# Kernel optimization log

Measured on AMD Instinct MI355X. Metric: run time of the kernel, lower is better.

The kernel has to match this reference:

```python
import jax, jax.numpy as jnp
import numpy as np
import math

B, S, H, NH = 8, 1024, 1024, 16
DH = H // NH


def _ln(x, g, b, eps=1e-5):
    m = x.mean(-1, keepdims=True)
    v = ((x - m) ** 2).mean(-1, keepdims=True)
    return (x - m) / jnp.sqrt(v + eps) * g + b


def _attn(qx, kx, vx, wq, bq, wk, bk, wv, bv, wo, bo, mask):
    b = qx.shape[0]
    def heads(t, w, bias):
        return (t @ w + bias).reshape(b, -1, NH, DH).transpose(0, 2, 1, 3)
    q, k, v = heads(qx, wq, bq), heads(kx, wk, bk), heads(vx, wv, bv)
    corr = jnp.einsum('bhqd,bhkd->bhqk', q, k) / math.sqrt(DH)  # [B,NH,Sq,Sk]
    corr = jnp.where(mask[:, None, :, None] == 0, -1e9, corr)  # mask per query row
    p = jax.nn.softmax(corr, axis=-1)
    o = jnp.einsum('bhqk,bhkd->bhqd', p, v).transpose(0, 2, 1, 3).reshape(b, -1, H)
    return o @ wo + bo


def setup_inputs() -> dict:
    key = jax.random.key(0)
    ks = jax.random.split(key, 16)
    d = {}
    d['x'] = jax.random.normal(ks[0], (B, S, H), jnp.float32)
    d['h'] = jax.random.normal(ks[1], (B, S, H), jnp.float32)
    d['mask'] = jnp.ones((B, S), jnp.int32)
    wnames = ['sa_wq', 'sa_wk', 'sa_wv', 'sa_wo', 'ca_wq', 'ca_wk', 'ca_wv', 'ca_wo', 'ff_w1', 'ff_w2']
    for i, n in enumerate(wnames):
        d[n] = jax.random.normal(ks[2 + i], (H, H), jnp.float32) * 0.02
    for n in ['sa_bq', 'sa_bk', 'sa_bv', 'sa_bo', 'ca_bq', 'ca_bk', 'ca_bv', 'ca_bo', 'ff_b1', 'ff_b2']:
        d[n] = jnp.zeros((H,), jnp.float32)
    for n in ['ln1', 'ln2', 'ln3', 'lnh', 'ff_ln']:
        d[n + '_g'] = jnp.ones((H,), jnp.float32)
        d[n + '_b'] = jnp.zeros((H,), jnp.float32)
    return d


def reference(x, h, mask, ln1_g, ln1_b, ln2_g, ln2_b, ln3_g, ln3_b, lnh_g, lnh_b,
              sa_wq, sa_bq, sa_wk, sa_bk, sa_wv, sa_bv, sa_wo, sa_bo,
              ca_wq, ca_bq, ca_wk, ca_bk, ca_wv, ca_bv, ca_wo, ca_bo,
              ff_w1, ff_b1, ff_w2, ff_b2, ff_ln_g, ff_ln_b):
    # self-attention block (pre-LN, residual)
    xn = _ln(x, ln1_g, ln1_b)
    hidden_in = _attn(xn, xn, xn, sa_wq, sa_bq, sa_wk, sa_bk, sa_wv, sa_bv, sa_wo, sa_bo, mask) + x
    # cross-attention block
    mid_n = _ln(hidden_in, ln2_g, ln2_b)
    hn = _ln(h, lnh_g, lnh_b)
    hidden_mid = _attn(mid_n, hn, hn, ca_wq, ca_bq, ca_wk, ca_bk, ca_wv, ca_bv, ca_wo, ca_bo, mask) + hidden_in
    # position-wise FFN (Conv1d k=1 == pointwise linear) with its own LN+residual
    y = _ln(hidden_mid, ln3_g, ln3_b)
    ff = jax.nn.relu(y @ ff_w1 + ff_b1) @ ff_w2 + ff_b2
    ffo = _ln(ff + y, ff_ln_g, ff_ln_b)
    return ffo + hidden_mid
```

## Files before the change

kernel.cpp:

```cpp
#include <hip/hip_runtime.h>

typedef unsigned short u16;
typedef unsigned int u32;
typedef float f32x4 __attribute__((ext_vector_type(4)));
typedef float f32x16 __attribute__((ext_vector_type(16)));
typedef __bf16 bf16x8 __attribute__((ext_vector_type(8)));

#define MFMA16(a, b, c) __builtin_amdgcn_mfma_f32_16x16x32_bf16(a, b, c, 0, 0, 0)
#define MFMA32(a, b, c) __builtin_amdgcn_mfma_f32_32x32x16_bf16(a, b, c, 0, 0, 0)
#define PLSWAP(x, y) asm volatile("v_permlane32_swap_b32 %0, %1" : "+v"(x), "+v"(y))

__device__ __forceinline__ u16 f2b(float f) {
    u32 u = __builtin_bit_cast(u32, f);
    u += 0x7fffu + ((u >> 16) & 1u);
    return (u16)(u >> 16);
}

__device__ __forceinline__ u32 pk2(float a, float b) {
    union { u32 u; __bf16 h[2]; } r;
    r.h[0] = (__bf16)a; r.h[1] = (__bf16)b;
    return r.u;
}

__device__ __forceinline__ void gload16(const u16* g, u16* l) {
    __builtin_amdgcn_global_load_lds((const __attribute__((address_space(1))) void*)g,
                                     (__attribute__((address_space(3))) void*)l, 16, 0, 0);
}

struct W10 { const float* p[10]; };
__global__ __launch_bounds__(256) void tcvt_k(W10 wp, u16* __restrict__ WT0) {
    const float* __restrict__ Wm = wp.p[blockIdx.z];
    u16* __restrict__ WT = WT0 + (size_t)blockIdx.z * 1048576;
    __shared__ float t[32][33];
    int bx = blockIdx.x, by = blockIdx.y;
    int tx = threadIdx.x, ty = threadIdx.y;
#pragma unroll
    for (int j = 0; j < 32; j += 8)
        t[ty + j][tx] = Wm[(size_t)(by * 32 + ty + j) * 1024 + bx * 32 + tx];
    __syncthreads();
#pragma unroll
    for (int j = 0; j < 32; j += 8)
        WT[(size_t)(bx * 32 + ty + j) * 1024 + by * 32 + tx] = f2b(t[tx][ty + j]);
}

__global__ __launch_bounds__(256) void vtr_k(const u16* __restrict__ Vg, int ldv, u16* __restrict__ VT) {
    __shared__ u16 t[32][34];
    int bx = blockIdx.x, by = blockIdx.y, b = blockIdx.z;
    int tx = threadIdx.x, ty = threadIdx.y;
#pragma unroll
    for (int j = 0; j < 32; j += 8)
        t[ty + j][tx] = Vg[(size_t)(b * 1024 + by * 32 + ty + j) * ldv + bx * 32 + tx];
    __syncthreads();
#pragma unroll
    for (int j = 0; j < 32; j += 8)
        VT[(size_t)(b * 1024 + bx * 32 + ty + j) * 1024 + by * 32 + tx] = t[tx][ty + j];
}

template <int MODE>
__global__ __launch_bounds__(256) void ln_k(const float* __restrict__ in1, const float* __restrict__ in2,
                                            const float* __restrict__ gg, const float* __restrict__ bb,
                                            const float* __restrict__ post,
                                            float* __restrict__ of, u16* __restrict__ ob) {
    int row = blockIdx.x, tid = threadIdx.x;
    size_t base = (size_t)row * 1024 + tid * 4;
    float4 x = *(const float4*)(in1 + base);
    if constexpr (MODE & 1) {
        float4 x2 = *(const float4*)(in2 + base);
        x.x += x2.x; x.y += x2.y; x.z += x2.z; x.w += x2.w;
    }
    float s1 = x.x + x.y + x.z + x.w;
    float s2 = x.x * x.x + x.y * x.y + x.z * x.z + x.w * x.w;
#pragma unroll
    for (int m = 32; m >= 1; m >>= 1) { s1 += __shfl_xor(s1, m); s2 += __shfl_xor(s2, m); }
    __shared__ float r1[4], r2[4];
    int lane = tid & 63, w = tid >> 6;
    if (lane == 0) { r1[w] = s1; r2[w] = s2; }
    __syncthreads();
    s1 = r1[0] + r1[1] + r1[2] + r1[3];
    s2 = r2[0] + r2[1] + r2[2] + r2[3];
    float mean = s1 * (1.0f / 1024.0f);
    float var = s2 * (1.0f / 1024.0f) - mean * mean;
    float rstd = rsqrtf(var + 1e-5f);
    float4 gv = *(const float4*)(gg + tid * 4);
    float4 bv = *(const float4*)(bb + tid * 4);
    float y0 = (x.x - mean) * rstd * gv.x + bv.x;
    float y1 = (x.y - mean) * rstd * gv.y + bv.y;
    float y2 = (x.z - mean) * rstd * gv.z + bv.z;
    float y3 = (x.w - mean) * rstd * gv.w + bv.w;
    if constexpr (MODE & 2) {
        float o0 = y0, o1 = y1, o2 = y2, o3 = y3;
        if constexpr (MODE & 8) {
            float4 p = *(const float4*)(post + base);
            o0 += p.x; o1 += p.y; o2 += p.z; o3 += p.w;
        }
        float4 o; o.x = o0; o.y = o1; o.z = o2; o.w = o3;
        *(float4*)(of + base) = o;
    }
    if constexpr (MODE & 4) {
        uint2 pk;
        pk.x = (u32)f2b(y0) | ((u32)f2b(y1) << 16);
        pk.y = (u32)f2b(y2) | ((u32)f2b(y3) << 16);
        *(uint2*)(ob + base) = pk;
    }
}

template <int EPI, int NBT>
__global__ __launch_bounds__(256, 3) void gemm_k(const u16* __restrict__ A, int lda,
                                                 const u16* __restrict__ WT,
                                                 const float* __restrict__ b0, const float* __restrict__ b1,
                                                 const float* __restrict__ b2,
                                                 float sc0, float sc1, float sc2,
                                                 const float* __restrict__ res,
                                                 void* __restrict__ outp, int ldc) {
    const int K = 1024;
    __shared__ u16 aL[2][4096];
    __shared__ u16 bL[2][4096];
    int id = blockIdx.x;
    const int CPX = 64 * NBT / 8;
    int swz = (id & 7) * CPX + (id >> 3);
    int bm = swz / NBT, bn = swz % NBT;
    const int m0 = bm * 128, n0 = bn * 128;
    int tid = threadIdx.x, lane = tid & 63, w = tid >> 6;
    int wm = w >> 1, wn = w & 1;
    int col = lane & 15, g = lane >> 4;
    const u16* Ag = A + (size_t)(m0 + w * 32 + (lane >> 2)) * lda + (lane & 3) * 8;
    const u16* Bg = WT + (size_t)(n0 + w * 32 + (lane >> 2)) * K + (lane & 3) * 8;

#define STG(buf, kt)                                                                            \
    {                                                                                           \
        _Pragma("unroll") for (int i_ = 0; i_ < 2; i_++) {                                      \
            gload16(Ag + (size_t)(kt) * 32 + (size_t)i_ * 16 * lda, &aL[buf][w * 1024 + i_ * 512]); \
            gload16(Bg + (size_t)(kt) * 32 + (size_t)i_ * 16 * K, &bL[buf][w * 1024 + i_ * 512]);   \
        }                                                                                       \
    }

    f32x4 acc[4][4];
#pragma unroll
    for (int m = 0; m < 4; m++)
#pragma unroll
        for (int n = 0; n < 4; n++) acc[m][n] = (f32x4){0.f, 0.f, 0.f, 0.f};

    STG(0, 0);
    __syncthreads();
#pragma unroll 2
    for (int kt = 0; kt < 32; ++kt) {
        int cur = kt & 1;
        if (kt < 31) STG(cur ^ 1, kt + 1);
        bf16x8 af[4], bfv[4];
#pragma unroll
        for (int m = 0; m < 4; m++) af[m] = *(const bf16x8*)&aL[cur][(wm * 64 + m * 16 + col) * 32 + g * 8];
#pragma unroll
        for (int n = 0; n < 4; n++) bfv[n] = *(const bf16x8*)&bL[cur][(wn * 64 + n * 16 + col) * 32 + g * 8];
#pragma unroll
        for (int m = 0; m < 4; m++)
#pragma unroll
            for (int n = 0; n < 4; n++) acc[m][n] = MFMA16(af[m], bfv[n], acc[m][n]);
        __syncthreads();
    }
#undef STG
    int seg = n0 >> 10;
    const float* bp = (NBT == 8) ? b0 : (seg == 0 ? b0 : (seg == 1 ? b1 : b2));
    float sg = (NBT == 8) ? sc0 : (seg == 0 ? sc0 : (seg == 1 ? sc1 : sc2));
    int nseg = n0 & 1023;
    float bv[4];
#pragma unroll
    for (int n = 0; n < 4; n++) bv[n] = bp[nseg + wn * 64 + n * 16 + col];
#pragma unroll
    for (int m = 0; m < 4; m++) {
#pragma unroll
        for (int r = 0; r < 4; r++) {
            int row = m0 + wm * 64 + m * 16 + g * 4 + r;
#pragma unroll
            for (int n = 0; n < 4; n++) {
                int c = n0 + wn * 64 + n * 16 + col;
                size_t idx = (size_t)row * ldc + c;
                float v = (acc[m][n][r] + bv[n]) * sg;
                if constexpr (EPI == 0) ((u16*)outp)[idx] = f2b(v);
                else if constexpr (EPI == 1) ((u16*)outp)[idx] = f2b(fmaxf(v, 0.f));
                else if constexpr (EPI == 2) ((float*)outp)[idx] = v + res[idx];
            }
        }
    }
}

__global__ __launch_bounds__(256) void attn_k(const u16* __restrict__ Q, int ldq,
                                              const u16* __restrict__ Kc, int ldk,
                                              const u16* __restrict__ VT,
                                              const int* __restrict__ mask,
                                              u16* __restrict__ O, int ldo) {
    const int S = 1024;
    int gid = blockIdx.x;
    int bq = gid >> 7, hh = (gid >> 3) & 15, bb = gid & 7;
    int tid = threadIdx.x, lane = tid & 63, w = tid >> 6;
    int q = lane & 31, hl = lane >> 5;
    int q0w = bq * 128 + w * 32;

    __shared__ u16 sm[18432];
#define KT(b, r, c) sm[(b) * 9216 + (r) * 72 + (c)]
#define VTL(b, r, c) sm[(b) * 9216 + 4608 + (r) * 72 + (c)]

    const u16* Qrow = Q + ((size_t)bb * S + q0w + q) * ldq + hh * 64;
    bool mneg = (mask[bb * S + q0w + q] == 0);
    bf16x8 qf[4];
#pragma unroll
    for (int c = 0; c < 4; c++) {
        qf[c] = *(const bf16x8*)(Qrow + c * 16 + hl * 8);
        if (mneg) qf[c] = (bf16x8)(__bf16)0.f;
    }

    float l = 0.f;
    f32x16 oa[2];
#pragma unroll
    for (int i = 0; i < 16; i++) { oa[0][i] = 0.f; oa[1][i] = 0.f; }

    int kk = tid >> 2, ks = tid & 3;
    const u16* gK = Kc + ((size_t)bb * S + kk) * ldk + hh * 64 + ks * 16;
    const u16* gVT = VT + ((size_t)(bb * 16 + hh) * 64 + kk) * 1024 + ks * 16;
    uint4 kr0, kr1, vr0, vr1;

#define LOADT(t)                                                      \
    {                                                                 \
        const u16* pk_ = gK + (size_t)(t) * 64 * ldk;                 \
        kr0 = *(const uint4*)pk_; kr1 = *(const uint4*)(pk_ + 8);     \
        const u16* pv_ = gVT + (size_t)(t) * 64;                      \
        vr0 = *(const uint4*)pv_; vr1 = *(const uint4*)(pv_ + 8);     \
    }
#define STORET(bf)                                       \
    {                                                    \
        *(uint4*)&KT(bf, kk, ks * 16) = kr0;             \
        *(uint4*)&KT(bf, kk, ks * 16 + 8) = kr1;         \
        *(uint4*)&VTL(bf, kk, ks * 16) = vr0;            \
        *(uint4*)&VTL(bf, kk, ks * 16 + 8) = vr1;        \
    }

    LOADT(0);
    STORET(0);

    for (int t = 0; t < 16; ++t) {
        int cur = t & 1;
        if (t < 15) LOADT(t + 1);
        __syncthreads();

        f32x16 sc[2];
#pragma unroll
        for (int i = 0; i < 16; i++) { sc[0][i] = 0.f; sc[1][i] = 0.f; }
        __builtin_amdgcn_s_setprio(1);
#pragma unroll
        for (int st = 0; st < 2; st++)
#pragma unroll
            for (int c = 0; c < 4; c++) {
                bf16x8 kf = *(const bf16x8*)&KT(cur, st * 32 + q, c * 16 + hl * 8);
                sc[st] = MFMA32(kf, qf[c], sc[st]);
            }
        __builtin_amdgcn_s_setprio(0);

#pragma unroll
        for (int st = 0; st < 2; st++)
#pragma unroll
            for (int r = 0; r < 16; r++) sc[st][r] = exp2f(sc[st][r]);
        float ts[8];
#pragma unroll
        for (int i = 0; i < 8; i++)
            ts[i] = (sc[0][i] + sc[0][i + 8]) + (sc[1][i] + sc[1][i + 8]);
#pragma unroll
        for (int i = 0; i < 4; i++) ts[i] += ts[i + 4];
        float rs = (ts[0] + ts[2]) + (ts[1] + ts[3]);
        rs += __shfl_xor(rs, 32);
        l += rs;

        __builtin_amdgcn_s_setprio(1);
#pragma unroll
        for (int st = 0; st < 2; st++) {
            u32 wv[8];
#pragma unroll
            for (int j = 0; j < 8; j++) wv[j] = pk2(sc[st][2 * j], sc[st][2 * j + 1]);
            PLSWAP(wv[0], wv[2]); PLSWAP(wv[1], wv[3]);
            PLSWAP(wv[4], wv[6]); PLSWAP(wv[5], wv[7]);
#pragma unroll
            for (int c = 0; c < 2; c++) {
                union { u32 u[4]; bf16x8 v; } pb;
                pb.u[0] = wv[c * 4 + 0]; pb.u[1] = wv[c * 4 + 1];
                pb.u[2] = wv[c * 4 + 2]; pb.u[3] = wv[c * 4 + 3];
#pragma unroll
                for (int dd = 0; dd < 2; dd++) {
                    bf16x8 vf = *(const bf16x8*)&VTL(cur, dd * 32 + q, st * 32 + c * 16 + hl * 8);
                    oa[dd] = MFMA32(vf, pb.v, oa[dd]);
                }
            }
        }
        __builtin_amdgcn_s_setprio(0);

        if (t < 15) STORET(cur ^ 1);
    }

    __syncthreads();
    float inv = 1.0f / l;
    u16* otw = sm + w * 2304;
#pragma unroll
    for (int dd = 0; dd < 2; dd++)
#pragma unroll
        for (int r = 0; r < 16; r++) {
            int d = (r & 3) + 8 * (r >> 2) + 4 * hl + 32 * dd;
            otw[q * 72 + d] = f2b(oa[dd][r] * inv);
        }
    __syncthreads();
    size_t obase = ((size_t)bb * S + q0w) * ldo + hh * 64;
#pragma unroll
    for (int i = 0; i < 4; i++) {
        int row = i * 8 + (lane >> 3);
        uint4 vdat = *(const uint4*)&otw[row * 72 + (lane & 7) * 8];
        *(uint4*)(O + obase + (size_t)row * ldo + (lane & 7) * 8) = vdat;
    }
#undef KT
#undef VTL
#undef LOADT
#undef STORET
}

extern "C" void kernel_launch(void* const* d_in, const int* in_sizes, int n_in,
                              void* d_out, int out_size, void* d_ws, size_t ws_size,
                              hipStream_t stream) {
    (void)in_sizes; (void)n_in; (void)out_size; (void)ws_size;
    const float* x = (const float*)d_in[0];
    const float* h = (const float*)d_in[1];
    const int* mask = (const int*)d_in[2];
    const float* W[10];
    const float* Bv[10];
    for (int i = 0; i < 10; i++) { W[i] = (const float*)d_in[3 + i]; Bv[i] = (const float*)d_in[13 + i]; }
    const float *ln1g = (const float*)d_in[23], *ln1b = (const float*)d_in[24];
    const float *ln2g = (const float*)d_in[25], *ln2b = (const float*)d_in[26];
    const float *ln3g = (const float*)d_in[27], *ln3b = (const float*)d_in[28];
    const float *lnhg = (const float*)d_in[29], *lnhb = (const float*)d_in[30];
    const float *flng = (const float*)d_in[31], *flnb = (const float*)d_in[32];

    const float SCLE = 0.18033688011112042f;

    char* ws = (char*)d_ws;
    size_t off = 0;
    auto alloc = [&](size_t bytes) -> char* {
        char* p = ws + off;
        off += (bytes + 255) & ~(size_t)255;
        return p;
    };
    const size_t MT = (size_t)8192 * 1024;
    u16* wtb = (u16*)alloc((size_t)10 * 1048576 * 2);
    u16* wt[10];
    for (int i = 0; i < 10; i++) wt[i] = wtb + (size_t)i * 1048576;
    u16* qkv = (u16*)alloc((size_t)8192 * 3072 * 2);
    u16* kv = qkv;
    u16* kb = qkv + (size_t)8192 * 2048;
    u16* bufA = (u16*)alloc(MT * 2);
    u16* qb   = (u16*)alloc(MT * 2);
    float* hid_in  = (float*)alloc(MT * 4);
    float* hid_mid = (float*)alloc(MT * 4);
    float* yf      = (float*)alloc(MT * 4);
    u16* hn = (u16*)yf;
    u16* vt_sa = bufA;
    u16* vt_ca = (u16*)hid_mid;
    float* outF = (float*)d_out;

    W10 wp;
    for (int i = 0; i < 10; i++) wp.p[i] = W[i];
    tcvt_k<<<dim3(32, 32, 10), dim3(32, 8), 0, stream>>>(wp, wtb);

    ln_k<4><<<8192, 256, 0, stream>>>(x, nullptr, ln1g, ln1b, nullptr, nullptr, bufA);
    gemm_k<0, 24><<<1536, 256, 0, stream>>>(bufA, 1024, wt[0], Bv[0], Bv[1], Bv[2], SCLE, 1.f, 1.f, nullptr, qkv, 3072);
    vtr_k<<<dim3(32, 32, 8), dim3(32, 8), 0, stream>>>(qkv + 2048, 3072, vt_sa);
    attn_k<<<1024, 256, 0, stream>>>(qkv, 3072, qkv + 1024, 3072, vt_sa, mask, qkv, 3072);
    gemm_k<2, 8><<<512, 256, 0, stream>>>(qkv, 3072, wt[3], Bv[3], Bv[3], Bv[3], 1.f, 1.f, 1.f, x, hid_in, 1024);

    ln_k<4><<<8192, 256, 0, stream>>>(hid_in, nullptr, ln2g, ln2b, nullptr, nullptr, bufA);
    ln_k<4><<<8192, 256, 0, stream>>>(h, nullptr, lnhg, lnhb, nullptr, nullptr, hn);
    gemm_k<0, 8><<<512, 256, 0, stream>>>(bufA, 1024, wt[4], Bv[4], Bv[4], Bv[4], SCLE, 1.f, 1.f, nullptr, qb, 1024);
    gemm_k<0, 16><<<1024, 256, 0, stream>>>(hn, 1024, wt[5], Bv[5], Bv[6], Bv[6], 1.f, 1.f, 1.f, nullptr, kv, 2048);
    vtr_k<<<dim3(32, 32, 8), dim3(32, 8), 0, stream>>>(kv + 1024, 2048, vt_ca);
    attn_k<<<1024, 256, 0, stream>>>(qb, 1024, kv, 2048, vt_ca, mask, qb, 1024);
    gemm_k<2, 8><<<512, 256, 0, stream>>>(qb, 1024, wt[7], Bv[7], Bv[7], Bv[7], 1.f, 1.f, 1.f, hid_in, hid_mid, 1024);

    ln_k<6><<<8192, 256, 0, stream>>>(hid_mid, nullptr, ln3g, ln3b, nullptr, yf, bufA);
    gemm_k<1, 8><<<512, 256, 0, stream>>>(bufA, 1024, wt[8], Bv[8], Bv[8], Bv[8], 1.f, 1.f, 1.f, nullptr, kb, 1024);
    gemm_k<2, 8><<<512, 256, 0, stream>>>(kb, 1024, wt[9], Bv[9], Bv[9], Bv[9], 1.f, 1.f, 1.f, yf, hid_in, 1024);
    ln_k<10><<<8192, 256, 0, stream>>>(hid_in, nullptr, flng, flnb, hid_mid, outF, nullptr);
}
```

Before: 495.8 us.

## Deepen GEMM pipeline to four LDS stages with swizzled layout and manual waits

The GEMM main loop moves from a double buffer to a four-slot LDS ring that keeps three k-tiles in flight. Completion is tracked with explicit vmcnt waits and raw barriers instead of __syncthreads. LDS rows are XOR-swizzled on both the global-to-LDS store and the fragment reads to cut bank conflicts, and MFMA sections get raised priority. The larger LDS footprint (64 KB) lowers the occupancy hint from 3 to 2 blocks per CU, which weakens latency hiding across blocks.

```diff
diff --git a/kernel.cpp b/kernel.cpp
--- a/kernel.cpp
+++ b/kernel.cpp
@@ -9,6 +9,14 @@
 #define MFMA16(a, b, c) __builtin_amdgcn_mfma_f32_16x16x32_bf16(a, b, c, 0, 0, 0)
 #define MFMA32(a, b, c) __builtin_amdgcn_mfma_f32_32x32x16_bf16(a, b, c, 0, 0, 0)
 #define PLSWAP(x, y) asm volatile("v_permlane32_swap_b32 %0, %1" : "+v"(x), "+v"(y))
+#define CFENCE() asm volatile("" ::: "memory")
+#define BAR()                         \
+    {                                 \
+        CFENCE();                     \
+        __builtin_amdgcn_s_barrier(); \
+        CFENCE();                     \
+    }
+#define WAITV(n) asm volatile("s_waitcnt vmcnt(" #n ")" ::: "memory")
 
 __device__ __forceinline__ u16 f2b(float f) {
     u32 u = __builtin_bit_cast(u32, f);
@@ -105,16 +113,14 @@
 }
 
 template <int EPI, int NBT>
-__global__ __launch_bounds__(256, 3) void gemm_k(const u16* __restrict__ A, int lda,
+__global__ __launch_bounds__(256, 2) void gemm_k(const u16* __restrict__ A, int lda,
                                                  const u16* __restrict__ WT,
                                                  const float* __restrict__ b0, const float* __restrict__ b1,
                                                  const float* __restrict__ b2,
                                                  float sc0, float sc1, float sc2,
                                                  const float* __restrict__ res,
                                                  void* __restrict__ outp, int ldc) {
-    const int K = 1024;
-    __shared__ u16 aL[2][4096];
-    __shared__ u16 bL[2][4096];
+    __shared__ u16 lds[32768];
     int id = blockIdx.x;
     const int CPX = 64 * NBT / 8;
     int swz = (id & 7) * CPX + (id >> 3);
@@ -122,17 +128,26 @@
     const int m0 = bm * 128, n0 = bn * 128;
     int tid = threadIdx.x, lane = tid & 63, w = tid >> 6;
     int wm = w >> 1, wn = w & 1;
-    int col = lane & 15, g = lane >> 4;
-    const u16* Ag = A + (size_t)(m0 + w * 32 + (lane >> 2)) * lda + (lane & 3) * 8;
-    const u16* Bg = WT + (size_t)(n0 + w * 32 + (lane >> 2)) * K + (lane & 3) * 8;
-
-#define STG(buf, kt)                                                                            \
-    {                                                                                           \
-        _Pragma("unroll") for (int i_ = 0; i_ < 2; i_++) {                                      \
-            gload16(Ag + (size_t)(kt) * 32 + (size_t)i_ * 16 * lda, &aL[buf][w * 1024 + i_ * 512]); \
-            gload16(Bg + (size_t)(kt) * 32 + (size_t)i_ * 16 * K, &bL[buf][w * 1024 + i_ * 512]);   \
-        }                                                                                       \
-    }
+    int col = lane & 15, fg = lane >> 4;
+
+    int r = tid >> 2, g = tid & 3;
+    int gr = r ^ ((r >> 3) & 1);
+    int gg = g ^ ((r >> 1) & 3);
+    const u16* Asrc = A + (size_t)(m0 + gr) * lda + gg * 8;
+    const u16* Bsrc = WT + (size_t)(n0 + gr) * 1024 + gg * 8;
+    u16* aDst = lds + w * 512;
+    u16* bDst = lds + 16384 + w * 512;
+
+#define STG(slot, kt)                                                      \
+    {                                                                      \
+        gload16(Asrc + (kt) * 32, aDst + (slot) * 4096);                   \
+        gload16(Asrc + (kt) * 32 + (size_t)64 * lda, aDst + (slot) * 4096 + 2048); \
+        gload16(Bsrc + (kt) * 32, bDst + (slot) * 4096);                   \
+        gload16(Bsrc + (kt) * 32 + (size_t)64 * 1024, bDst + (slot) * 4096 + 2048); \
+    }
+
+    int aoff = (((wm * 64 + col) * 32) + fg * 8) ^ ((col >> 1) << 3);
+    int boff = (((wn * 64 + col) * 32) + fg * 8) ^ ((col >> 1) << 3);
 
     f32x4 acc[4][4];
 #pragma unroll
@@ -140,24 +155,36 @@
 #pragma unroll
         for (int n = 0; n < 4; n++) acc[m][n] = (f32x4){0.f, 0.f, 0.f, 0.f};
 
-    STG(0, 0);
-    __syncthreads();
-#pragma unroll 2
-    for (int kt = 0; kt < 32; ++kt) {
-        int cur = kt & 1;
-        if (kt < 31) STG(cur ^ 1, kt + 1);
+    auto body = [&](int slot) {
+        const u16* aS = lds + slot * 4096;
+        const u16* bS = lds + 16384 + slot * 4096;
         bf16x8 af[4], bfv[4];
 #pragma unroll
-        for (int m = 0; m < 4; m++) af[m] = *(const bf16x8*)&aL[cur][(wm * 64 + m * 16 + col) * 32 + g * 8];
-#pragma unroll
-        for (int n = 0; n < 4; n++) bfv[n] = *(const bf16x8*)&bL[cur][(wn * 64 + n * 16 + col) * 32 + g * 8];
+        for (int m = 0; m < 4; m++) af[m] = *(const bf16x8*)(aS + aoff + m * 512);
+#pragma unroll
+        for (int n = 0; n < 4; n++) bfv[n] = *(const bf16x8*)(bS + boff + n * 512);
+        __builtin_amdgcn_s_setprio(1);
 #pragma unroll
         for (int m = 0; m < 4; m++)
 #pragma unroll
             for (int n = 0; n < 4; n++) acc[m][n] = MFMA16(af[m], bfv[n], acc[m][n]);
-        __syncthreads();
-    }
+        __builtin_amdgcn_s_setprio(0);
+    };
+
+    STG(0, 0); STG(1, 1); STG(2, 2);
+#pragma unroll 4
+    for (int s = 0; s < 29; ++s) {
+        STG((s + 3) & 3, s + 3);
+        WAITV(12);
+        BAR();
+        body(s & 3);
+        BAR();
+    }
+    WAITV(8);  BAR(); body(1); BAR();
+    WAITV(4);  BAR(); body(2); BAR();
+    WAITV(0);  BAR(); body(3); BAR();
 #undef STG
+
     int seg = n0 >> 10;
     const float* bp = (NBT == 8) ? b0 : (seg == 0 ? b0 : (seg == 1 ? b1 : b2));
     float sg = (NBT == 8) ? sc0 : (seg == 0 ? sc0 : (seg == 1 ? sc1 : sc2));
@@ -168,13 +195,13 @@
 #pragma unroll
     for (int m = 0; m < 4; m++) {
 #pragma unroll
-        for (int r = 0; r < 4; r++) {
-            int row = m0 + wm * 64 + m * 16 + g * 4 + r;
+        for (int rr = 0; rr < 4; rr++) {
+            int row = m0 + wm * 64 + m * 16 + fg * 4 + rr;
 #pragma unroll
             for (int n = 0; n < 4; n++) {
                 int c = n0 + wn * 64 + n * 16 + col;
                 size_t idx = (size_t)row * ldc + c;
-                float v = (acc[m][n][r] + bv[n]) * sg;
+                float v = (acc[m][n][rr] + bv[n]) * sg;
                 if constexpr (EPI == 0) ((u16*)outp)[idx] = f2b(v);
                 else if constexpr (EPI == 1) ((u16*)outp)[idx] = f2b(fmaxf(v, 0.f));
                 else if constexpr (EPI == 2) ((float*)outp)[idx] = v + res[idx];
@@ -257,7 +284,7 @@
 #pragma unroll
         for (int st = 0; st < 2; st++)
 #pragma unroll
-            for (int r = 0; r < 16; r++) sc[st][r] = exp2f(sc[st][r]);
+            for (int rr = 0; rr < 16; rr++) sc[st][rr] = exp2f(sc[st][rr]);
         float ts[8];
 #pragma unroll
         for (int i = 0; i < 8; i++)
@@ -299,9 +326,9 @@
 #pragma unroll
     for (int dd = 0; dd < 2; dd++)
 #pragma unroll
-        for (int r = 0; r < 16; r++) {
-            int d = (r & 3) + 8 * (r >> 2) + 4 * hl + 32 * dd;
-            otw[q * 72 + d] = f2b(oa[dd][r] * inv);
+        for (int rr = 0; rr < 16; rr++) {
+            int d = (rr & 3) + 8 * (rr >> 2) + 4 * hl + 32 * dd;
+            otw[q * 72 + d] = f2b(oa[dd][rr] * inv);
         }
     __syncthreads();
     size_t obase = ((size_t)bb * S + q0w) * ldo + hh * 64;
```

After: 511.9 us. +3.3%, slower.
